# Kernel tuning notes

Measured on AMD Instinct MI355X. Metric: run time of the kernel, lower is better.

The kernel has to match this reference:

```python
import jax, jax.numpy as jnp
import numpy as np

N = 100000      # nodes
E = 1600000     # edges (avg degree 16)
IN_DIM = 64
OUT_DIM = 128
BN_EPS = 1e-5


def setup_inputs() -> dict:
    key = jax.random.key(0)
    kx, ke, kw, kb, ks = jax.random.split(key, 5)
    x = jax.random.normal(kx, (N, IN_DIM), dtype=jnp.float32)
    edge_index = jax.random.randint(ke, (2, E), 0, N, dtype=jnp.int32)
    # GCNConv linear weight (no bias inside lin; conv bias separate)
    W = jax.random.normal(kw, (IN_DIM, OUT_DIM), dtype=jnp.float32) / np.sqrt(IN_DIM)
    bias = jax.random.normal(kb, (OUT_DIM,), dtype=jnp.float32) * 0.01
    # skip projection Linear(in_dim, out_dim, bias=False)
    skip_W = jax.random.normal(ks, (IN_DIM, OUT_DIM), dtype=jnp.float32) / np.sqrt(IN_DIM)
    # BatchNorm1d affine params (training-mode batch stats used in forward)
    gamma = jnp.ones((OUT_DIM,), dtype=jnp.float32)
    beta = jnp.zeros((OUT_DIM,), dtype=jnp.float32)
    return {"x": x, "edge_index": edge_index, "W": W, "bias": bias,
            "skip_W": skip_W, "gamma": gamma, "beta": beta}


def _gcn_forward(x, edge_index, W, bias, skip_W, gamma, beta):
    n = x.shape[0]
    # GCNConv, normalize=True, add_self_loops=True (PyG defaults)
    row, col = edge_index[0], edge_index[1]
    loop = jnp.arange(n, dtype=edge_index.dtype)
    row_f = jnp.concatenate([row, loop])   # source nodes
    col_f = jnp.concatenate([col, loop])   # target nodes

    xt = x @ W                             # [N, OUT]
    deg = jax.ops.segment_sum(jnp.ones_like(col_f, dtype=xt.dtype), col_f,
                              num_segments=n)          # >= 1 due to self loops
    dinv = jax.lax.rsqrt(deg)
    norm = dinv[row_f] * dinv[col_f]                    # [E+N]
    msgs = xt[row_f] * norm[:, None]                    # gather + scale
    out = jax.ops.segment_sum(msgs, col_f, num_segments=n) + bias

    # skip-sum (in_dim != out_dim -> project)
    out = out + x @ skip_W

    # BatchNorm1d (training-mode batch statistics), affine
    mean = out.mean(axis=0)
    var = out.var(axis=0)
    out = (out - mean) * jax.lax.rsqrt(var + BN_EPS) * gamma + beta

    # ReLU; dropout p=0.0 -> identity
    return jax.nn.relu(out)


def reference(x, edge_index, W, bias, skip_W, gamma, beta):
    return _gcn_forward(x, edge_index, W, bias, skip_W, gamma, beta)
```

## Files before the change

kernel.cpp:

```cpp
#include <hip/hip_runtime.h>


typedef unsigned short ushort;
typedef __bf16 bf16x8 __attribute__((ext_vector_type(8)));
typedef float f32x4 __attribute__((ext_vector_type(4)));
typedef float f32x2 __attribute__((ext_vector_type(2)));

constexpr int N_NODES = 100000;
constexpr int N_PAD   = 100096;
constexpr int E_EDGES = 1600000;

constexpr int BUCK_SHIFT = 7;
constexpr int NBUCK   = (N_NODES + 127) / 128;
constexpr int NBUCK_P = 784;
constexpr int CHUNK   = 4096;
constexpr int NCHUNK  = (E_EDGES + CHUNK - 1) / CHUNK;
constexpr int SORT_CAP = 4096;

constexpr size_t OFF_SCALE  = 0;
constexpr size_t OFF_DINV   = 256;
constexpr size_t OFF_ROWPTR = 100352;
constexpr size_t OFF_BASE   = 200480;
constexpr size_t OFF_GHIST  = 201280;
constexpr size_t OFF_PART   = OFF_GHIST;
constexpr size_t OFF_BINNED = 507824;
constexpr size_t OFF_XB     = 2107824;
constexpr size_t OFF_U      = 5310896;
constexpr size_t OFF_PRE    = 8513968;
constexpr size_t OFF_XD8    = OFF_PRE;
constexpr size_t OFF_BT     = 14920112;

static __device__ __forceinline__ ushort f2bf(float f) {
    union { float f; unsigned u; } v; v.f = f;
    unsigned r = v.u + 0x7FFFu + ((v.u >> 16) & 1u);
    return (ushort)(r >> 16);
}
static __device__ __forceinline__ float bf2f(ushort u) {
    union { unsigned u; float f; } v; v.u = (unsigned)u << 16;
    return v.f;
}
static __device__ __forceinline__ unsigned pack_fp8x4(float a, float b, float c, float d) {
    int r = 0;
    r = __builtin_amdgcn_cvt_pk_fp8_f32(a, b, r, false);
    r = __builtin_amdgcn_cvt_pk_fp8_f32(c, d, r, true);
    return (unsigned)r;
}

__global__ __launch_bounds__(256) void k_hist(const int* __restrict__ col,
                                              int* __restrict__ gh,
                                              const float* __restrict__ W,
                                              const float* __restrict__ skipW,
                                              ushort* __restrict__ Bt) {
    int c = blockIdx.x, t = threadIdx.x;
    if (c >= NCHUNK) {
        int idx = (c - NCHUNK) * 256 + t;
        int k = idx >> 7, n = idx & 127;
        float v = (k < 64) ? W[k * 128 + n] : skipW[(k - 64) * 128 + n];
        Bt[n * 128 + k] = f2bf(v);
        return;
    }
    __shared__ int h[NBUCK_P];
    for (int b = t; b < NBUCK_P; b += 256) h[b] = 0;
    __syncthreads();
    const int4* col4 = (const int4*)col;
    int g0 = c * (CHUNK / 4);
#pragma unroll
    for (int i = 0; i < CHUNK / 1024; ++i) {
        int g4 = g0 + i * 256 + t;
        if (g4 * 4 + 3 < E_EDGES) {
            int4 cc = col4[g4];
            atomicAdd(&h[cc.x >> BUCK_SHIFT], 1);
            atomicAdd(&h[cc.y >> BUCK_SHIFT], 1);
            atomicAdd(&h[cc.z >> BUCK_SHIFT], 1);
            atomicAdd(&h[cc.w >> BUCK_SHIFT], 1);
        } else {
#pragma unroll
            for (int j = 0; j < 4; ++j) {
                int e = g4 * 4 + j;
                if (e < E_EDGES) atomicAdd(&h[col[e] >> BUCK_SHIFT], 1);
            }
        }
    }
    __syncthreads();
    for (int b = t; b < NBUCK_P; b += 256) gh[c * NBUCK_P + b] = h[b];
}

__global__ __launch_bounds__(512) void k_scan_buckets(int* __restrict__ gh,
                                                      int* __restrict__ base) {
    __shared__ int lds[512];
    int b = blockIdx.x, t = threadIdx.x;
    int v = (t < NCHUNK) ? gh[t * NBUCK_P + b] : 0;
    lds[t] = v;
    __syncthreads();
    int val = v;
#pragma unroll
    for (int off = 1; off < 512; off <<= 1) {
        int add = (t >= off) ? lds[t - off] : 0;
        __syncthreads();
        val += add;
        lds[t] = val;
        __syncthreads();
    }
    if (t < NCHUNK) gh[t * NBUCK_P + b] = val - v;
    if (t == 511) base[b] = val;
}

__global__ __launch_bounds__(1024) void k_scan_bases(int* __restrict__ base,
                                                     int* __restrict__ rowptr) {
    __shared__ int lds[1024];
    int t = threadIdx.x;
    int v = (t < NBUCK) ? base[t] : 0;
    lds[t] = v;
    __syncthreads();
    int val = v;
#pragma unroll
    for (int off = 1; off < 1024; off <<= 1) {
        int add = (t >= off) ? lds[t - off] : 0;
        __syncthreads();
        val += add;
        lds[t] = val;
        __syncthreads();
    }
    if (t < NBUCK) base[t] = val - v;
    if (t == 1023) {
        base[NBUCK] = val;
        rowptr[N_NODES] = val;
    }
}

__global__ __launch_bounds__(256) void k_scatter_bin(const int* __restrict__ row,
                                                     const int* __restrict__ col,
                                                     const int* __restrict__ gh,
                                                     const int* __restrict__ base,
                                                     unsigned int* __restrict__ binned) {
    __shared__ int cur[NBUCK_P];
    int c = blockIdx.x, t = threadIdx.x;
    for (int b = t; b < NBUCK_P; b += 256) {
        int bb = (b < NBUCK) ? base[b] : 0;
        cur[b] = bb + gh[c * NBUCK_P + b];
    }
    __syncthreads();
    const int4* col4 = (const int4*)col;
    const int4* row4 = (const int4*)row;
    int g0 = c * (CHUNK / 4);
#pragma unroll
    for (int i = 0; i < CHUNK / 1024; ++i) {
        int g4 = g0 + i * 256 + t;
        if (g4 * 4 + 3 < E_EDGES) {
            int4 cc = col4[g4];
            int4 rr = row4[g4];
            int p;
            p = atomicAdd(&cur[cc.x >> BUCK_SHIFT], 1);
            binned[p] = ((unsigned)(cc.x & 127) << 17) | (unsigned)rr.x;
            p = atomicAdd(&cur[cc.y >> BUCK_SHIFT], 1);
            binned[p] = ((unsigned)(cc.y & 127) << 17) | (unsigned)rr.y;
            p = atomicAdd(&cur[cc.z >> BUCK_SHIFT], 1);
            binned[p] = ((unsigned)(cc.z & 127) << 17) | (unsigned)rr.z;
            p = atomicAdd(&cur[cc.w >> BUCK_SHIFT], 1);
            binned[p] = ((unsigned)(cc.w & 127) << 17) | (unsigned)rr.w;
        } else {
#pragma unroll
            for (int j = 0; j < 4; ++j) {
                int e = g4 * 4 + j;
                if (e < E_EDGES) {
                    int d = col[e], s = row[e];
                    int p = atomicAdd(&cur[d >> BUCK_SHIFT], 1);
                    binned[p] = ((unsigned)(d & 127) << 17) | (unsigned)s;
                }
            }
        }
    }
}

__global__ __launch_bounds__(256) void k_sortbucket(unsigned int* __restrict__ binned,
                                                    const int* __restrict__ base,
                                                    int* __restrict__ rowptr,
                                                    float* __restrict__ dinv,
                                                    const float* __restrict__ x,
                                                    ushort* __restrict__ xb,
                                                    unsigned* __restrict__ xd8) {
    __shared__ unsigned int ebuf[SORT_CAP];
    __shared__ int sbuf[SORT_CAP];
    __shared__ int lcnt[128];
    __shared__ int lptr[128];
    __shared__ float ldinv[128];
    __shared__ int wsum[2];
    int b = blockIdx.x, t = threadIdx.x;
    int i0 = base[b], i1 = base[b + 1];
    int cnt = i1 - i0;
    if (cnt > SORT_CAP) cnt = SORT_CAP;
    int n0 = b << BUCK_SHIFT;
    int nn = min(128, N_NODES - n0);

    for (int k = t; k < cnt; k += 256) ebuf[k] = binned[i0 + k];
    if (t < 128) lcnt[t] = 0;
    __syncthreads();
    for (int k = t; k < cnt; k += 256) atomicAdd(&lcnt[ebuf[k] >> 17], 1);
    __syncthreads();

    int myc = 0, val = 0;
    if (t < 128) {
        myc = lcnt[t];
        val = myc;
#pragma unroll
        for (int d = 1; d < 64; d <<= 1) {
            int o = __shfl_up(val, d);
            if ((t & 63) >= d) val += o;
        }
        if ((t & 63) == 63) wsum[t >> 6] = val;
    }
    __syncthreads();
    if (t < 128) {
        if (t >= 64) val += wsum[0];
        int excl = val - myc;
        lptr[t] = excl;
        float dv = rsqrtf((float)myc + 1.0f);
        ldinv[t] = dv;
        if (t < nn) {
            rowptr[n0 + t] = i0 + excl;
            dinv[n0 + t] = dv;
        }
    }
    __syncthreads();
    for (int k = t; k < cnt; k += 256) {
        unsigned int e = ebuf[k];
        int j = (int)(e >> 17);
        int p = atomicAdd(&lptr[j], 1);
        sbuf[p] = (int)(e & 0x1FFFF);
    }
    __syncthreads();
    for (int k = t; k < cnt; k += 256) binned[i0 + k] = (unsigned int)sbuf[k];

#pragma unroll
    for (int it = 0; it < 8; ++it) {
        int idx = it * 256 + t;
        int nl = idx >> 4, q = idx & 15;
        int c = n0 + nl;
        ushort4 bb = {0, 0, 0, 0};
        unsigned w8 = 0;
        if (nl < nn) {
            float4 v = ((const float4*)x)[(size_t)c * 16 + q];
            bb.x = f2bf(v.x); bb.y = f2bf(v.y); bb.z = f2bf(v.z); bb.w = f2bf(v.w);
            float d = ldinv[nl];
            w8 = pack_fp8x4(v.x * d, v.y * d, v.z * d, v.w * d);
        }
        ((ushort4*)xb)[(size_t)c * 16 + q] = bb;
        xd8[(size_t)c * 16 + q] = w8;
    }
}

__global__ __launch_bounds__(256) void k_agg(const unsigned* __restrict__ xd8,
                                             const float* __restrict__ dinv,
                                             const int* __restrict__ rowptr,
                                             const unsigned int* __restrict__ csr,
                                             ushort* __restrict__ u) {
    int t = blockIdx.x * blockDim.x + threadIdx.x;
    if (t >= N_PAD * 16) return;
    int c = t >> 4;
    int q = t & 15;
    if (c >= N_NODES) {
        ushort4 z = {0, 0, 0, 0};
        ((ushort4*)u)[t] = z;
        return;
    }
    float dc = dinv[c];
    float4 acc;
    {
        unsigned w = xd8[t];
        f32x2 lo = __builtin_amdgcn_cvt_pk_f32_fp8((int)w, false);
        f32x2 hi = __builtin_amdgcn_cvt_pk_f32_fp8((int)w, true);
        acc.x = lo.x; acc.y = lo.y; acc.z = hi.x; acc.w = hi.y;
    }
    int i0 = rowptr[c], i1 = rowptr[c + 1];
    int i = i0;
    for (; i + 8 <= i1; i += 8) {
        int s[8];
#pragma unroll
        for (int k = 0; k < 8; ++k) s[k] = (int)csr[i + k];
        unsigned w[8];
#pragma unroll
        for (int k = 0; k < 8; ++k) w[k] = xd8[s[k] * 16 + q];
#pragma unroll
        for (int k = 0; k < 8; ++k) {
            f32x2 lo = __builtin_amdgcn_cvt_pk_f32_fp8((int)w[k], false);
            f32x2 hi = __builtin_amdgcn_cvt_pk_f32_fp8((int)w[k], true);
            acc.x += lo.x; acc.y += lo.y; acc.z += hi.x; acc.w += hi.y;
        }
    }
    for (; i < i1; ++i) {
        unsigned w = xd8[(int)csr[i] * 16 + q];
        f32x2 lo = __builtin_amdgcn_cvt_pk_f32_fp8((int)w, false);
        f32x2 hi = __builtin_amdgcn_cvt_pk_f32_fp8((int)w, true);
        acc.x += lo.x; acc.y += lo.y; acc.z += hi.x; acc.w += hi.y;
    }
    ushort4 o;
    o.x = f2bf(acc.x * dc); o.y = f2bf(acc.y * dc);
    o.z = f2bf(acc.z * dc); o.w = f2bf(acc.w * dc);
    ((ushort4*)u)[t] = o;
}

__global__ __launch_bounds__(256) void k_gemm(const ushort* __restrict__ u,
                                              const ushort* __restrict__ xb,
                                              const ushort* __restrict__ Bt,
                                              const float* __restrict__ bias,
                                              ushort* __restrict__ pre,
                                              float* __restrict__ partial) {
    __shared__ float sred[128];
    __shared__ float qred[128];
    int tid = threadIdx.x;
    int wave = tid >> 6, lane = tid & 63;
    int wm = wave >> 1, wn = wave & 1;
    int l15 = lane & 15, quad = lane >> 4;
    int row0 = blockIdx.x * 128 + wm * 64;
    int col0 = wn * 64;

    if (tid < 128) { sred[tid] = 0.f; qred[tid] = 0.f; }
    __syncthreads();

    bf16x8 af[4][4], bf_[4][4];
#pragma unroll
    for (int kc = 0; kc < 4; ++kc) {
        const ushort* abase = (kc < 2) ? u : xb;
        int ko = (kc & 1) * 32 + quad * 8;
#pragma unroll
        for (int im = 0; im < 4; ++im)
            af[kc][im] = *(const bf16x8*)&abase[(size_t)(row0 + im * 16 + l15) * 64 + ko];
#pragma unroll
        for (int jn = 0; jn < 4; ++jn)
            bf_[kc][jn] = *(const bf16x8*)&Bt[(size_t)(col0 + jn * 16 + l15) * 128 + kc * 32 + quad * 8];
    }

    f32x4 acc[4][4];
#pragma unroll
    for (int a = 0; a < 4; ++a)
#pragma unroll
        for (int b = 0; b < 4; ++b) acc[a][b] = (f32x4){0.f, 0.f, 0.f, 0.f};

#pragma unroll
    for (int kc = 0; kc < 4; ++kc)
#pragma unroll
        for (int im = 0; im < 4; ++im)
#pragma unroll
            for (int jn = 0; jn < 4; ++jn)
                acc[im][jn] = __builtin_amdgcn_mfma_f32_16x16x32_bf16(
                    af[kc][im], bf_[kc][jn], acc[im][jn], 0, 0, 0);

    int coln[4];
    float bi[4];
#pragma unroll
    for (int jn = 0; jn < 4; ++jn) {
        coln[jn] = col0 + jn * 16 + l15;
        bi[jn] = bias[coln[jn]];
    }
    float lsum[4] = {0.f, 0.f, 0.f, 0.f};
    float lsq[4]  = {0.f, 0.f, 0.f, 0.f};
#pragma unroll
    for (int im = 0; im < 4; ++im) {
        int rbase = row0 + im * 16 + quad * 4;
#pragma unroll
        for (int r = 0; r < 4; ++r) {
            int rowi = rbase + r;
            if (rowi < N_NODES) {
#pragma unroll
                for (int jn = 0; jn < 4; ++jn) {
                    float v = acc[im][jn][r] + bi[jn];
                    pre[(size_t)rowi * 128 + coln[jn]] = f2bf(v);
                    lsum[jn] += v;
                    lsq[jn]  += v * v;
                }
            }
        }
    }
#pragma unroll
    for (int jn = 0; jn < 4; ++jn) {
        atomicAdd(&sred[coln[jn]], lsum[jn]);
        atomicAdd(&qred[coln[jn]], lsq[jn]);
    }
    __syncthreads();
    if (tid < 128) {
        partial[(size_t)blockIdx.x * 256 + tid]       = sred[tid];
        partial[(size_t)blockIdx.x * 256 + 128 + tid] = qred[tid];
    }
}

__global__ __launch_bounds__(256) void k_reduce(const float* __restrict__ partial,
                                                const float* __restrict__ gamma,
                                                const float* __restrict__ beta,
                                                float* __restrict__ scaleshift) {
    __shared__ float ls[256], lq[256];
    int j = blockIdx.x;
    int t = threadIdx.x;
    float s = 0.f, q = 0.f;
    for (int p = t; p < NBUCK; p += 256) {
        s += partial[(size_t)p * 256 + j];
        q += partial[(size_t)p * 256 + 128 + j];
    }
    ls[t] = s; lq[t] = q;
    __syncthreads();
#pragma unroll
    for (int off = 128; off > 0; off >>= 1) {
        if (t < off) { ls[t] += ls[t + off]; lq[t] += lq[t + off]; }
        __syncthreads();
    }
    if (t == 0) {
        float mean = ls[0] * (1.0f / N_NODES);
        float var  = lq[0] * (1.0f / N_NODES) - mean * mean;
        float sc   = gamma[j] * rsqrtf(var + 1e-5f);
        scaleshift[j]       = sc;
        scaleshift[128 + j] = beta[j] - mean * sc;
    }
}

__global__ void k_apply(const ushort* __restrict__ pre, float* __restrict__ out,
                        const float* __restrict__ scaleshift) {
    int t = blockIdx.x * blockDim.x + threadIdx.x;
    if (t >= N_NODES * 32) return;
    int j4 = t & 31;
    ushort4 p = ((const ushort4*)pre)[t];
    float4 sc = ((const float4*)scaleshift)[j4];
    float4 sh = ((const float4*)(scaleshift + 128))[j4];
    float4 v;
    v.x = fmaxf(fmaf(bf2f(p.x), sc.x, sh.x), 0.f);
    v.y = fmaxf(fmaf(bf2f(p.y), sc.y, sh.y), 0.f);
    v.z = fmaxf(fmaf(bf2f(p.z), sc.z, sh.z), 0.f);
    v.w = fmaxf(fmaf(bf2f(p.w), sc.w, sh.w), 0.f);
    ((float4*)out)[t] = v;
}

extern "C" void kernel_launch(void* const* d_in, const int* in_sizes, int n_in,
                              void* d_out, int out_size, void* d_ws, size_t ws_size,
                              hipStream_t stream) {
    const float* x      = (const float*)d_in[0];
    const int*   eidx   = (const int*)d_in[1];
    const float* W      = (const float*)d_in[2];
    const float* bias   = (const float*)d_in[3];
    const float* skipW  = (const float*)d_in[4];
    const float* gamma  = (const float*)d_in[5];
    const float* beta   = (const float*)d_in[6];
    float* out = (float*)d_out;
    float* ws  = (float*)d_ws;

    const int* row = eidx;
    const int* col = eidx + E_EDGES;

    float* scaleshift = ws + OFF_SCALE;
    float* dinv       = ws + OFF_DINV;
    int*   rowptr     = (int*)(ws + OFF_ROWPTR);
    int*   base       = (int*)(ws + OFF_BASE);
    int*   gh         = (int*)(ws + OFF_GHIST);
    float* partial    = ws + OFF_PART;
    unsigned int* binned = (unsigned int*)(ws + OFF_BINNED);
    ushort* xb        = (ushort*)(ws + OFF_XB);
    ushort* u         = (ushort*)(ws + OFF_U);
    unsigned* xd8     = (unsigned*)(ws + OFF_XD8);
    ushort* pre       = (ushort*)(ws + OFF_PRE);
    ushort* Bt        = (ushort*)(ws + OFF_BT);

    k_hist<<<NCHUNK + 64, 256, 0, stream>>>(col, gh, W, skipW, Bt);
    k_scan_buckets<<<NBUCK, 512, 0, stream>>>(gh, base);
    k_scan_bases<<<1, 1024, 0, stream>>>(base, rowptr);
    k_scatter_bin<<<NCHUNK, 256, 0, stream>>>(row, col, gh, base, binned);
    k_sortbucket<<<NBUCK, 256, 0, stream>>>(binned, base, rowptr, dinv, x, xb, xd8);
    k_agg<<<(N_PAD * 16 + 255) / 256, 256, 0, stream>>>(xd8, dinv, rowptr, binned, u);
    k_gemm<<<NBUCK, 256, 0, stream>>>(u, xb, Bt, bias, pre, partial);
    k_reduce<<<128, 256, 0, stream>>>(partial, gamma, beta, scaleshift);
    k_apply<<<(N_NODES * 32 + 255) / 256, 256, 0, stream>>>(pre, out, scaleshift);
}
```

Measured before the change: 217.4 us.

## Transpose chunk histogram with wave-level scan and drop bf16 x copy

Chunk size doubles, which halves the number of histogram chunks. The per-chunk bucket histogram is now stored bucket-major, so one wave can scan each bucket's chunk counts with shuffles instead of a 512-thread LDS scan per bucket. The bf16 copy of x written in the sort kernel is removed, and the GEMM instead loads x as fp32 and converts it to bf16 in registers. This saves a global write and read of xb, but GEMM A-loads double in size for that half, and fewer, larger chunks may reduce parallelism in the hist and scatter kernels.

```diff
diff --git a/kernel.cpp b/kernel.cpp
--- a/kernel.cpp
+++ b/kernel.cpp
@@ -13,8 +13,9 @@
 constexpr int BUCK_SHIFT = 7;
 constexpr int NBUCK   = (N_NODES + 127) / 128;
 constexpr int NBUCK_P = 784;
-constexpr int CHUNK   = 4096;
+constexpr int CHUNK   = 8192;
 constexpr int NCHUNK  = (E_EDGES + CHUNK - 1) / CHUNK;
+constexpr int GH_STRIDE = 200;
 constexpr int SORT_CAP = 4096;
 
 constexpr size_t OFF_SCALE  = 0;
@@ -22,13 +23,12 @@
 constexpr size_t OFF_ROWPTR = 100352;
 constexpr size_t OFF_BASE   = 200480;
 constexpr size_t OFF_GHIST  = 201280;
-constexpr size_t OFF_PART   = OFF_GHIST;
-constexpr size_t OFF_BINNED = 507824;
-constexpr size_t OFF_XB     = 2107824;
-constexpr size_t OFF_U      = 5310896;
-constexpr size_t OFF_PRE    = 8513968;
+constexpr size_t OFF_BINNED = 358080;
+constexpr size_t OFF_PART   = OFF_BINNED;
+constexpr size_t OFF_U      = 1958080;
+constexpr size_t OFF_PRE    = 5161152;
 constexpr size_t OFF_XD8    = OFF_PRE;
-constexpr size_t OFF_BT     = 14920112;
+constexpr size_t OFF_BT     = 11567296;
 
 static __device__ __forceinline__ ushort f2bf(float f) {
     union { float f; unsigned u; } v; v.f = f;
@@ -45,9 +45,15 @@
     r = __builtin_amdgcn_cvt_pk_fp8_f32(c, d, r, true);
     return (unsigned)r;
 }
+static __device__ __forceinline__ bf16x8 pack_bf8(float4 a, float4 b) {
+    union { ushort us[8]; bf16x8 v; } u;
+    u.us[0] = f2bf(a.x); u.us[1] = f2bf(a.y); u.us[2] = f2bf(a.z); u.us[3] = f2bf(a.w);
+    u.us[4] = f2bf(b.x); u.us[5] = f2bf(b.y); u.us[6] = f2bf(b.z); u.us[7] = f2bf(b.w);
+    return u.v;
+}
 
 __global__ __launch_bounds__(256) void k_hist(const int* __restrict__ col,
-                                              int* __restrict__ gh,
+                                              int* __restrict__ gh_t,
                                               const float* __restrict__ W,
                                               const float* __restrict__ skipW,
                                               ushort* __restrict__ Bt) {
@@ -82,27 +88,30 @@
         }
     }
     __syncthreads();
-    for (int b = t; b < NBUCK_P; b += 256) gh[c * NBUCK_P + b] = h[b];
-}
-
-__global__ __launch_bounds__(512) void k_scan_buckets(int* __restrict__ gh,
-                                                      int* __restrict__ base) {
-    __shared__ int lds[512];
-    int b = blockIdx.x, t = threadIdx.x;
-    int v = (t < NCHUNK) ? gh[t * NBUCK_P + b] : 0;
-    lds[t] = v;
-    __syncthreads();
-    int val = v;
-#pragma unroll
-    for (int off = 1; off < 512; off <<= 1) {
-        int add = (t >= off) ? lds[t - off] : 0;
-        __syncthreads();
-        val += add;
-        lds[t] = val;
-        __syncthreads();
-    }
-    if (t < NCHUNK) gh[t * NBUCK_P + b] = val - v;
-    if (t == 511) base[b] = val;
+    for (int b = t; b < NBUCK_P; b += 256) gh_t[(size_t)b * GH_STRIDE + c] = h[b];
+}
+
+__global__ __launch_bounds__(256) void k_scan_chunks(int* __restrict__ gh_t,
+                                                     int* __restrict__ base) {
+    int w = threadIdx.x >> 6, l = threadIdx.x & 63;
+    int b = blockIdx.x * 4 + w;
+    if (b >= NBUCK_P) return;
+    int* rowp = gh_t + (size_t)b * GH_STRIDE;
+    int carry = 0;
+#pragma unroll
+    for (int i = 0; i < 4; ++i) {
+        int idx = i * 64 + l;
+        int v = (idx < NCHUNK) ? rowp[idx] : 0;
+        int orig = v;
+#pragma unroll
+        for (int d = 1; d < 64; d <<= 1) {
+            int o = __shfl_up(v, d);
+            if (l >= d) v += o;
+        }
+        if (idx < NCHUNK) rowp[idx] = carry + v - orig;
+        carry += __shfl(v, 63);
+    }
+    if (l == 0 && b < NBUCK) base[b] = carry;
 }
 
 __global__ __launch_bounds__(1024) void k_scan_bases(int* __restrict__ base,
@@ -130,14 +139,14 @@
 
 __global__ __launch_bounds__(256) void k_scatter_bin(const int* __restrict__ row,
                                                      const int* __restrict__ col,
-                                                     const int* __restrict__ gh,
+                                                     const int* __restrict__ gh_t,
                                                      const int* __restrict__ base,
                                                      unsigned int* __restrict__ binned) {
     __shared__ int cur[NBUCK_P];
     int c = blockIdx.x, t = threadIdx.x;
     for (int b = t; b < NBUCK_P; b += 256) {
         int bb = (b < NBUCK) ? base[b] : 0;
-        cur[b] = bb + gh[c * NBUCK_P + b];
+        cur[b] = bb + gh_t[(size_t)b * GH_STRIDE + c];
     }
     __syncthreads();
     const int4* col4 = (const int4*)col;
@@ -177,7 +186,6 @@
                                                     int* __restrict__ rowptr,
                                                     float* __restrict__ dinv,
                                                     const float* __restrict__ x,
-                                                    ushort* __restrict__ xb,
                                                     unsigned* __restrict__ xd8) {
     __shared__ unsigned int ebuf[SORT_CAP];
     __shared__ int sbuf[SORT_CAP];
@@ -236,15 +244,12 @@
         int idx = it * 256 + t;
         int nl = idx >> 4, q = idx & 15;
         int c = n0 + nl;
-        ushort4 bb = {0, 0, 0, 0};
         unsigned w8 = 0;
         if (nl < nn) {
             float4 v = ((const float4*)x)[(size_t)c * 16 + q];
-            bb.x = f2bf(v.x); bb.y = f2bf(v.y); bb.z = f2bf(v.z); bb.w = f2bf(v.w);
             float d = ldinv[nl];
             w8 = pack_fp8x4(v.x * d, v.y * d, v.z * d, v.w * d);
         }
-        ((ushort4*)xb)[(size_t)c * 16 + q] = bb;
         xd8[(size_t)c * 16 + q] = w8;
     }
 }
@@ -300,7 +305,7 @@
 }
 
 __global__ __launch_bounds__(256) void k_gemm(const ushort* __restrict__ u,
-                                              const ushort* __restrict__ xb,
+                                              const float* __restrict__ x,
                                               const ushort* __restrict__ Bt,
                                               const float* __restrict__ bias,
                                               ushort* __restrict__ pre,
@@ -319,16 +324,32 @@
 
     bf16x8 af[4][4], bf_[4][4];
 #pragma unroll
-    for (int kc = 0; kc < 4; ++kc) {
-        const ushort* abase = (kc < 2) ? u : xb;
-        int ko = (kc & 1) * 32 + quad * 8;
+    for (int kc = 0; kc < 2; ++kc) {
+        int ko = kc * 32 + quad * 8;
 #pragma unroll
         for (int im = 0; im < 4; ++im)
-            af[kc][im] = *(const bf16x8*)&abase[(size_t)(row0 + im * 16 + l15) * 64 + ko];
+            af[kc][im] = *(const bf16x8*)&u[(size_t)(row0 + im * 16 + l15) * 64 + ko];
+    }
+#pragma unroll
+    for (int kc = 2; kc < 4; ++kc) {
+        int ko = (kc - 2) * 32 + quad * 8;
+#pragma unroll
+        for (int im = 0; im < 4; ++im) {
+            int r = row0 + im * 16 + l15;
+            float4 v0 = make_float4(0.f, 0.f, 0.f, 0.f);
+            float4 v1 = v0;
+            if (r < N_NODES) {
+                v0 = *(const float4*)&x[(size_t)r * 64 + ko];
+                v1 = *(const float4*)&x[(size_t)r * 64 + ko + 4];
+            }
+            af[kc][im] = pack_bf8(v0, v1);
+        }
+    }
+#pragma unroll
+    for (int kc = 0; kc < 4; ++kc)
 #pragma unroll
         for (int jn = 0; jn < 4; ++jn)
             bf_[kc][jn] = *(const bf16x8*)&Bt[(size_t)(col0 + jn * 16 + l15) * 128 + kc * 32 + quad * 8];
-    }
 
     f32x4 acc[4][4];
 #pragma unroll
@@ -447,22 +468,21 @@
     float* dinv       = ws + OFF_DINV;
     int*   rowptr     = (int*)(ws + OFF_ROWPTR);
     int*   base       = (int*)(ws + OFF_BASE);
-    int*   gh         = (int*)(ws + OFF_GHIST);
+    int*   gh_t       = (int*)(ws + OFF_GHIST);
+    unsigned int* binned = (unsigned int*)(ws + OFF_BINNED);
     float* partial    = ws + OFF_PART;
-    unsigned int* binned = (unsigned int*)(ws + OFF_BINNED);
-    ushort* xb        = (ushort*)(ws + OFF_XB);
     ushort* u         = (ushort*)(ws + OFF_U);
     unsigned* xd8     = (unsigned*)(ws + OFF_XD8);
     ushort* pre       = (ushort*)(ws + OFF_PRE);
     ushort* Bt        = (ushort*)(ws + OFF_BT);
 
-    k_hist<<<NCHUNK + 64, 256, 0, stream>>>(col, gh, W, skipW, Bt);
-    k_scan_buckets<<<NBUCK, 512, 0, stream>>>(gh, base);
+    k_hist<<<NCHUNK + 64, 256, 0, stream>>>(col, gh_t, W, skipW, Bt);
+    k_scan_chunks<<<(NBUCK_P + 3) / 4, 256, 0, stream>>>(gh_t, base);
     k_scan_bases<<<1, 1024, 0, stream>>>(base, rowptr);
-    k_scatter_bin<<<NCHUNK, 256, 0, stream>>>(row, col, gh, base, binned);
-    k_sortbucket<<<NBUCK, 256, 0, stream>>>(binned, base, rowptr, dinv, x, xb, xd8);
+    k_scatter_bin<<<NCHUNK, 256, 0, stream>>>(row, col, gh_t, base, binned);
+    k_sortbucket<<<NBUCK, 256, 0, stream>>>(binned, base, rowptr, dinv, x, xd8);
     k_agg<<<(N_PAD * 16 + 255) / 256, 256, 0, stream>>>(xd8, dinv, rowptr, binned, u);
-    k_gemm<<<NBUCK, 256, 0, stream>>>(u, xb, Bt, bias, pre, partial);
+    k_gemm<<<NBUCK, 256, 0, stream>>>(u, x, Bt, bias, pre, partial);
     k_reduce<<<128, 256, 0, stream>>>(partial, gamma, beta, scaleshift);
     k_apply<<<(N_NODES * 32 + 255) / 256, 256, 0, stream>>>(pre, out, scaleshift);
 }
```

Result: faster. 208.4 us (median of 2 runs) (-4.2%).
